# Kernel tuning notes

Hardware: AMD Instinct MI355X
Metric: run time of the kernel (lower is better)

## Reference

```python
import jax, jax.numpy as jnp
import numpy as np

N_LIG = 1024; K = 32; N = N_LIG * K; KNN = 8; E = N * KNN
IN_F = 16; T_F = 16; HID = 128; OUT_F = 64; DEPTH = 4; NG = 20; NT = 1000
EDGE_IN = NG + T_F  # 36
NORM_FACTOR = 5.0

# GaussianSmearing constants (type_='exp', start=0, stop=4, num_gaussians=20)
_off = np.exp(np.linspace(np.log(1.0), np.log(5.0), NG)) - 1.0
_d = np.diff(_off); _d = np.concatenate([_d[:1], _d])
GS_OFFSET = jnp.asarray(_off, jnp.float32)
GS_COEFF = jnp.asarray(-0.5 / _d ** 2, jnp.float32)


def _layernorm(v, g, b, eps=1e-5):
    mu = v.mean(-1, keepdims=True)
    var = ((v - mu) ** 2).mean(-1, keepdims=True)
    return (v - mu) / jnp.sqrt(var + eps) * g + b


def setup_inputs() -> dict:
    rng = np.random.default_rng(0)
    key = jax.random.key(0)
    ks = jax.random.split(key, 24)
    x = jax.random.uniform(ks[0], (N, 3), jnp.float32)   # keeps all sq-dists < 7
    h = jax.random.normal(ks[1], (N, IN_F), jnp.float32)
    t = jax.random.randint(ks[2], (N,), 0, NT, jnp.int32)
    t_bond = jax.random.randint(ks[3], (N_LIG * K * (K - 1),), 0, NT, jnp.int32)
    batch_ligand = (jnp.arange(N) // K).astype(jnp.int32)
    # knn-like edges restricted to each ligand (no self loops)
    i_local = np.arange(N) % K
    j = rng.integers(0, K, size=(N, KNN))
    j = np.where(j == i_local[:, None], (j + 1) % K, j)
    col = (np.arange(N) // K * K)[:, None] + j
    row = np.repeat(np.arange(N), KNN)
    edges = jnp.asarray(np.stack([row, col.reshape(-1)]), jnp.int32)

    def lin(k, fi, fo):
        return jax.random.normal(k, (fi, fo), jnp.float32) / np.sqrt(fi)

    def stk(k, fi, fo):
        return jax.random.normal(k, (DEPTH, fi, fo), jnp.float32) / np.sqrt(fi)

    inp = dict(x=x, h=h, t=t, edges=edges, t_bond=t_bond, batch_ligand=batch_ligand,
               num_atoms_per_ligand=K, num_ligands=N_LIG)
    inp['time_emb_table'] = 0.02 * jax.random.normal(ks[4], (NT, T_F), jnp.float32)
    inp['W_in'] = lin(ks[5], IN_F + T_F, HID); inp['b_in'] = jnp.zeros((HID,), jnp.float32)
    inp['gcl_We1'] = stk(ks[6], 2 * HID + EDGE_IN, HID); inp['gcl_be1'] = jnp.zeros((DEPTH, HID), jnp.float32)
    inp['gcl_g1'] = jnp.ones((DEPTH, HID), jnp.float32); inp['gcl_bt1'] = jnp.zeros((DEPTH, HID), jnp.float32)
    inp['gcl_We2'] = stk(ks[7], HID, HID); inp['gcl_be2'] = jnp.zeros((DEPTH, HID), jnp.float32)
    inp['gcl_Watt'] = stk(ks[8], HID, 1); inp['gcl_batt'] = jnp.zeros((DEPTH, 1), jnp.float32)
    inp['gcl_Wn1'] = stk(ks[9], 2 * HID, HID); inp['gcl_bn1'] = jnp.zeros((DEPTH, HID), jnp.float32)
    inp['gcl_g2'] = jnp.ones((DEPTH, HID), jnp.float32); inp['gcl_bt2'] = jnp.zeros((DEPTH, HID), jnp.float32)
    inp['gcl_Wn2'] = stk(ks[10], HID, HID); inp['gcl_bn2'] = jnp.zeros((DEPTH, HID), jnp.float32)
    inp['W_oe'] = lin(ks[11], HID, OUT_F); inp['b_oe'] = jnp.zeros((OUT_F,), jnp.float32)
    inp['W_f'] = lin(ks[12], OUT_F, 1); inp['b_f'] = jnp.zeros((1,), jnp.float32)
    return inp


def _forward(x, h, time_emb_table, W_in, b_in, gcl_We1, gcl_be1, gcl_g1, gcl_bt1,
             gcl_We2, gcl_be2, gcl_Watt, gcl_batt, gcl_Wn1, gcl_bn1, gcl_g2, gcl_bt2,
             gcl_Wn2, gcl_bn2, W_oe, b_oe, W_f, b_f,
             t, edges, t_bond, batch_ligand, num_atoms_per_ligand, num_ligands):
    n_nodes = x.shape[0]
    row, col = edges[0], edges[1]
    # h <- cat(h, time_emb)
    hh = jnp.concatenate([h, time_emb_table[t]], axis=-1)
    # distances + Gaussian smearing (all edges pass the <7 filter by construction)
    cdiff = x[row] - x[col]                          # [E,3]
    radial = jnp.sum(cdiff ** 2, axis=1)             # [E]
    dist = jnp.clip(jnp.sqrt(radial), 0.0, 4.0)
    dd = dist[:, None] - GS_OFFSET[None, :]
    smear = jnp.exp(GS_COEFF * dd * dd)              # [E,NG]
    Kc = num_atoms_per_ligand
    sbi = row * (Kc - 1) + col - (row // Kc) * Kc - (row < col).astype(row.dtype)
    edge_attr = jnp.concatenate([time_emb_table[t_bond[sbi]], smear], axis=-1)  # [E,36]
    hh = hh @ W_in + b_in                            # [N,HID]
    for l in range(DEPTH):
        # edge model: gather -> MLP(LN, SiLU) -> sigmoid attention gate
        m = jnp.concatenate([hh[row], hh[col], edge_attr], axis=-1)
        m = jax.nn.silu(_layernorm(m @ gcl_We1[l] + gcl_be1[l], gcl_g1[l], gcl_bt1[l]))
        mij = jax.nn.silu(m @ gcl_We2[l] + gcl_be2[l])
        att = jax.nn.sigmoid(mij @ gcl_Watt[l] + gcl_batt[l])
        ef = mij * att                               # [E,HID]
        # node model: scatter-add aggregate (sum / normalization_factor) -> MLP -> residual
        agg = jax.ops.segment_sum(ef, row, num_segments=n_nodes) / NORM_FACTOR
        nm = jnp.concatenate([hh, agg], axis=-1)
        nm = jax.nn.silu(_layernorm(nm @ gcl_Wn1[l] + gcl_bn1[l], gcl_g2[l], gcl_bt2[l]))
        hh = hh + (nm @ gcl_Wn2[l] + gcl_bn2[l])
    ho = hh @ W_oe + b_oe                            # [N,OUT_F]
    counts = jax.ops.segment_sum(jnp.ones((n_nodes,), ho.dtype), batch_ligand, num_segments=num_ligands)
    pooled = jax.ops.segment_sum(ho, batch_ligand, num_segments=num_ligands) / counts[:, None]
    return (pooled @ W_f + b_f).squeeze(-1)          # [num_ligands]


def reference(x, h, t, edges, t_bond, batch_ligand, num_atoms_per_ligand, num_ligands,
              time_emb_table, W_in, b_in, gcl_We1, gcl_be1, gcl_g1, gcl_bt1,
              gcl_We2, gcl_be2, gcl_Watt, gcl_batt, gcl_Wn1, gcl_bn1, gcl_g2, gcl_bt2,
              gcl_Wn2, gcl_bn2, W_oe, b_oe, W_f, b_f):
    return _forward(x, h, time_emb_table, W_in, b_in, gcl_We1, gcl_be1, gcl_g1, gcl_bt1,
                    gcl_We2, gcl_be2, gcl_Watt, gcl_batt, gcl_Wn1, gcl_bn1, gcl_g2, gcl_bt2,
                    gcl_Wn2, gcl_bn2, W_oe, b_oe, W_f, b_f,
                    t, edges, t_bond, batch_ligand, num_atoms_per_ligand, num_ligands)
```

## Files before the change

### kernel.cpp

```cpp
#include <hip/hip_runtime.h>
#include <math.h>

#define NNODES 32768
#define NLIG   1024
#define KAT    32
#define KNN    8
#define NEDGES (NNODES*KNN)
#define HID    128
#define TF     16
#define NG     20
#define OUTF   64

#define NPB    16
#define EPB    128
#define K1     320
#define MIDSTR 132

typedef unsigned short u16;
typedef _Float16 f16;
typedef __attribute__((__ext_vector_type__(8))) _Float16 f16x8;
typedef __attribute__((__ext_vector_type__(4))) float f32x4;

union U8h { f16 a[8]; f16x8 v; };

__device__ const float GS_OG[20] = {
    0.0f, 0.0883984f, 0.1845966f, 0.2893285f, 0.4033028f,
    0.5273539f, 0.6623701f, 0.8093209f, 0.9692606f, 1.1433389f,
    1.3328075f, 1.5390240f, 1.7634662f, 2.0077560f, 2.2736369f,
    2.5630207f, 2.8779861f, 3.2207938f, 3.5939058f, 4.0f };
__device__ const float GS_CF[20] = {
    -63.9853f, -63.9853f, -54.0303f, -45.5840f, -38.4908f,
    -32.4913f, -27.4283f, -23.1540f, -19.5460f, -16.4999f,
    -13.9282f, -11.7577f, -9.92569f, -8.37837f, -7.07287f,
    -5.97065f, -5.04016f, -4.25470f, -3.59163f, -3.03191f };

__device__ __forceinline__ float siluf(float v) {
    return __fdividef(v, 1.0f + __expf(-v));
}
__device__ __forceinline__ float sigf(float v) {
    return __fdividef(1.0f, 1.0f + __expf(-v));
}
__device__ __forceinline__ f32x4 mfma16(f16x8 a, f16x8 b, f32x4 c) {
    return __builtin_amdgcn_mfma_f32_16x16x32_f16(a, b, c, 0, 0, 0);
}

#define PREP_TEMB 16000
#define PREP_W1   (4*128*K1)
#define PREP_W2   (4*128*128)
#define PREP_WN1  (4*128*256)
#define PREP_WN2  (4*128*128)
#define PREP_TOT  (PREP_TEMB+PREP_W1+PREP_W2+PREP_WN1+PREP_WN2)

__global__ __launch_bounds__(256) void prep_k(
    const float* __restrict__ temb, const float* __restrict__ We1,
    const float* __restrict__ We2,  const float* __restrict__ Wn1,
    const float* __restrict__ Wn2,
    f16* __restrict__ tembF,
    f16* __restrict__ W1T, f16* __restrict__ W2T,
    f16* __restrict__ WN1T, f16* __restrict__ WN2T)
{
    int i = blockIdx.x*256 + threadIdx.x;
    if (i >= PREP_TOT) return;
    float v; f16* dst; int di;
    if (i < PREP_TEMB) {
        v = temb[i]; dst = tembF; di = i;
    } else if (i < PREP_TEMB + PREP_W1) {
        int j = i - PREP_TEMB; di = j; dst = W1T;
        int l = j / (128*K1); int r = j - l*(128*K1);
        int col = r / K1, k = r - col*K1;
        v = (k < 292) ? We1[(size_t)l*292*128 + (size_t)k*128 + col] : 0.0f;
    } else if (i < PREP_TEMB + PREP_W1 + PREP_W2) {
        int j = i - PREP_TEMB - PREP_W1; di = j; dst = W2T;
        int l = j >> 14; int r = j & 16383;
        int col = r >> 7, k = r & 127;
        v = We2[(size_t)l*16384 + (size_t)k*128 + col];
    } else if (i < PREP_TEMB + PREP_W1 + PREP_W2 + PREP_WN1) {
        int j = i - PREP_TEMB - PREP_W1 - PREP_W2; di = j; dst = WN1T;
        int l = j >> 15; int r = j & 32767;
        int col = r >> 8, k = r & 255;
        v = Wn1[(size_t)l*32768 + (size_t)k*128 + col];
    } else {
        int j = i - PREP_TEMB - PREP_W1 - PREP_W2 - PREP_WN1; di = j; dst = WN2T;
        int l = j >> 14; int r = j & 16383;
        int col = r >> 7, k = r & 127;
        v = Wn2[(size_t)l*16384 + (size_t)k*128 + col];
    }
    dst[di] = (f16)v;
}

__global__ __launch_bounds__(256) void embed_k(
    const float* __restrict__ h, const int* __restrict__ t,
    const float* __restrict__ temb, const float* __restrict__ Win,
    const float* __restrict__ bin, float* __restrict__ hh,
    f16* __restrict__ hhF)
{
    __shared__ float sIn[8][32];
    const int tid = threadIdx.x;
    {
        const int n = tid >> 5, i = tid & 31;
        const int node = blockIdx.x*8 + n;
        sIn[n][i] = (i < TF) ? h[node*TF + i] : temb[t[node]*TF + (i-TF)];
    }
    __syncthreads();
    const int sub = tid >> 7, col = tid & 127;
    float acc[4];
    const float b = bin[col];
    acc[0]=acc[1]=acc[2]=acc[3]=b;
    #pragma unroll 8
    for (int i = 0; i < 32; ++i) {
        const float wv = Win[i*HID + col];
        acc[0] = fmaf(sIn[sub][i],   wv, acc[0]);
        acc[1] = fmaf(sIn[2+sub][i], wv, acc[1]);
        acc[2] = fmaf(sIn[4+sub][i], wv, acc[2]);
        acc[3] = fmaf(sIn[6+sub][i], wv, acc[3]);
    }
    #pragma unroll
    for (int nn = 0; nn < 4; ++nn) {
        const size_t idx = (size_t)(blockIdx.x*8 + nn*2 + sub)*HID + col;
        hh[idx] = acc[nn];
        hhF[idx] = (f16)acc[nn];
    }
}

__global__ __launch_bounds__(256, 3) void edge_k(
    const f16* __restrict__ hhF, const float* __restrict__ x,
    const int* __restrict__ ecol, const int* __restrict__ tbond,
    const f16* __restrict__ tembF,
    const f16* __restrict__ W1T, const f16* __restrict__ W2T,
    const float* __restrict__ be1, const float* __restrict__ g1,
    const float* __restrict__ bt1, const float* __restrict__ be2,
    const float* __restrict__ Watt, const float* __restrict__ batt,
    f16* __restrict__ aggF)
{
    __shared__ __align__(16) char smem[38400];
    f16*   tbl   = (f16*)(smem);
    f16*   tailB = (f16*)(smem + 8192);
    float* sStats= (float*)(smem + 32768);
    float* sMuInv= (float*)(smem + 36864);
    f16*   sB2   = (f16*)(smem);
    float* sAP   = (float*)(smem + 32768);
    float* sAttv = (float*)(smem + 37888);

    const int tid = threadIdx.x;
    const int node0 = blockIdx.x * NPB;
    const int ligBase = node0 & ~31;
    const int aBase   = node0 & 31;
    const int w = tid >> 6, lane = tid & 63, lr = lane & 15, lh = lane >> 4;
    const int colB0 = w*32 + lr, colB1 = colB0 + 16;

    unsigned aColPk0 = 0, aColPk1 = 0;
    #pragma unroll
    for (int rt = 0; rt < 4; ++rt)
        aColPk0 |= (unsigned)(ecol[node0*KNN + rt*16 + lr] & 31) << (rt*8);
    #pragma unroll
    for (int rt = 0; rt < 4; ++rt)
        aColPk1 |= (unsigned)(ecol[node0*KNN + (4+rt)*16 + lr] & 31) << (rt*8);

    const f16* bF0 = W1T + (size_t)colB0*K1 + lh*8;
    const f16* bF1 = W1T + (size_t)colB1*K1 + lh*8;
    f16x8 wf0 = *(const f16x8*)bF0, wf1 = *(const f16x8*)bF1;

    for (int idx = tid; idx < 512; idx += 256) {
        const int a = idx >> 4, c4 = idx & 15;
        const f16x8 v = *(const f16x8*)(hhF + (size_t)(ligBase + a)*HID + c4*8);
        *(f16x8*)&tbl[a*128 + ((c4 ^ (a & 15)) << 3)] = v;
    }

    for (int pe = tid; pe < 1024; pe += 256) {
        const int row = pe & 127, part = pe >> 7;
        U8h vh;
        if (part < 2) {
            const int r = node0 + (row >> 3);
            const int c = ecol[node0*KNN + row];
            int sbi = r*(KAT-1) + c - (r/KAT)*KAT - (r < c ? 1 : 0);
            const int tb = tbond[sbi];
            #pragma unroll
            for (int j = 0; j < 8; ++j)
                vh.a[j] = tembF[tb*TF + part*8 + j];
        } else if (part < 5) {
            const int r = node0 + (row >> 3);
            const int c = ecol[node0*KNN + row];
            float dx = x[3*r]-x[3*c], dy = x[3*r+1]-x[3*c+1], dz = x[3*r+2]-x[3*c+2];
            float dist = fminf(sqrtf(dx*dx+dy*dy+dz*dz), 4.0f);
            #pragma unroll
            for (int j = 0; j < 8; ++j) {
                int g = (part-2)*8 + j;
                float v = 0.0f;
                if (g < NG) {
                    float dd = dist - GS_OG[g];
                    v = __expf(GS_CF[g]*dd*dd);
                }
                vh.a[j] = (f16)v;
            }
        } else {
            #pragma unroll
            for (int j = 0; j < 8; ++j) vh.a[j] = (f16)0.0f;
        }
        *(f16x8*)&tailB[row*64 + ((part ^ (row & 7)) << 3)] = vh.v;
    }
    __syncthreads();

    f32x4 acc[8][2];
    #pragma unroll
    for (int rt = 0; rt < 8; ++rt) { acc[rt][0] = (f32x4){0,0,0,0}; acc[rt][1] = (f32x4){0,0,0,0}; }
    {
        #pragma unroll
        for (int s = 0; s < 10; ++s) {
            f16x8 nf0 = wf0, nf1 = wf1;
            if (s < 9) {
                nf0 = *(const f16x8*)(bF0 + 32*(s+1));
                nf1 = *(const f16x8*)(bF1 + 32*(s+1));
            }
            if (s < 4) {
                #pragma unroll
                for (int rt = 0; rt < 8; ++rt) {
                    const int aR = aBase + 2*rt + (lr >> 3);
                    const int c4 = s*4 + lh;
                    const int ad = aR*128 + ((c4 ^ (aR & 15)) << 3);
                    const f16x8 ah = *(const f16x8*)&tbl[ad];
                    acc[rt][0] = mfma16(ah, wf0, acc[rt][0]);
                    acc[rt][1] = mfma16(ah, wf1, acc[rt][1]);
                }
            } else if (s < 8) {
                #pragma unroll
                for (int rt = 0; rt < 8; ++rt) {
                    const int aC = (int)((rt < 4 ? (aColPk0 >> (rt*8))
                                                 : (aColPk1 >> ((rt-4)*8))) & 31u);
                    const int c4 = (s-4)*4 + lh;
                    const int ad = aC*128 + ((c4 ^ (aC & 15)) << 3);
                    const f16x8 ah = *(const f16x8*)&tbl[ad];
                    acc[rt][0] = mfma16(ah, wf0, acc[rt][0]);
                    acc[rt][1] = mfma16(ah, wf1, acc[rt][1]);
                }
            } else {
                #pragma unroll
                for (int rt = 0; rt < 8; ++rt) {
                    const int r = rt*16 + lr;
                    const int c = (s-8)*4 + lh;
                    const int ad = r*64 + ((c ^ (r & 7)) << 3);
                    const f16x8 ah = *(const f16x8*)&tailB[ad];
                    acc[rt][0] = mfma16(ah, wf0, acc[rt][0]);
                    acc[rt][1] = mfma16(ah, wf1, acc[rt][1]);
                }
            }
            wf0 = nf0; wf1 = nf1;
        }
    }

    {
        const float b10 = be1[colB0], b11 = be1[colB1];
        #pragma unroll
        for (int rt = 0; rt < 8; ++rt)
            #pragma unroll
            for (int j = 0; j < 4; ++j) { acc[rt][0][j] += b10; acc[rt][1][j] += b11; }
    }
    {
        #pragma unroll
        for (int rt = 0; rt < 8; ++rt) {
            float sv[4], qv[4];
            #pragma unroll
            for (int j = 0; j < 4; ++j) {
                const float a0 = acc[rt][0][j], a1 = acc[rt][1][j];
                sv[j] = a0 + a1; qv[j] = a0*a0 + a1*a1;
            }
            #pragma unroll
            for (int msk = 1; msk < 16; msk <<= 1) {
                #pragma unroll
                for (int j = 0; j < 4; ++j) {
                    sv[j] += __shfl_xor(sv[j], msk);
                    qv[j] += __shfl_xor(qv[j], msk);
                }
            }
            if (lr == 0) {
                #pragma unroll
                for (int j = 0; j < 4; ++j) {
                    const int row = rt*16 + 4*lh + j;
                    sStats[(row*4 + w)*2 + 0] = sv[j];
                    sStats[(row*4 + w)*2 + 1] = qv[j];
                }
            }
        }
    }
    __syncthreads();

    if (tid < EPB) {
        const float4 a = *(const float4*)&sStats[tid*8];
        const float4 b = *(const float4*)&sStats[tid*8 + 4];
        const float st = a.x + a.z + b.x + b.z;
        const float qt = a.y + a.w + b.y + b.w;
        const float mu  = st * (1.0f/HID);
        const float var = qt * (1.0f/HID) - mu*mu;
        sMuInv[tid*2 + 0] = mu;
        sMuInv[tid*2 + 1] = rsqrtf(var + 1e-5f);
    }
    __syncthreads();

    const f16* c2F0 = W2T + (size_t)colB0*HID + lh*8;
    const f16* c2F1 = W2T + (size_t)colB1*HID + lh*8;
    f16x8 g2f0 = *(const f16x8*)c2F0, g2f1 = *(const f16x8*)c2F1;

    {
        const float G0 = g1[colB0], G1s = g1[colB1];
        const float B0 = bt1[colB0], B1s = bt1[colB1];
        #pragma unroll
        for (int rt = 0; rt < 8; ++rt) {
            const int r0 = rt*16 + 4*lh;
            const float4 mi0 = *(const float4*)&sMuInv[r0*2];
            const float4 mi1 = *(const float4*)&sMuInv[r0*2 + 4];
            acc[rt][0][0] = siluf(fmaf((acc[rt][0][0]-mi0.x)*mi0.y, G0, B0));
            acc[rt][1][0] = siluf(fmaf((acc[rt][1][0]-mi0.x)*mi0.y, G1s, B1s));
            acc[rt][0][1] = siluf(fmaf((acc[rt][0][1]-mi0.z)*mi0.w, G0, B0));
            acc[rt][1][1] = siluf(fmaf((acc[rt][1][1]-mi0.z)*mi0.w, G1s, B1s));
            acc[rt][0][2] = siluf(fmaf((acc[rt][0][2]-mi1.x)*mi1.y, G0, B0));
            acc[rt][1][2] = siluf(fmaf((acc[rt][1][2]-mi1.x)*mi1.y, G1s, B1s));
            acc[rt][0][3] = siluf(fmaf((acc[rt][0][3]-mi1.z)*mi1.w, G0, B0));
            acc[rt][1][3] = siluf(fmaf((acc[rt][1][3]-mi1.z)*mi1.w, G1s, B1s));
        }
    }
    {
        #pragma unroll
        for (int rt = 0; rt < 8; ++rt) {
            #pragma unroll
            for (int hcol = 0; hcol < 2; ++hcol) {
                const int col = hcol ? colB1 : colB0;
                const int gch = col >> 3, cw = col & 7;
                #pragma unroll
                for (int j = 0; j < 4; ++j) {
                    const int row = rt*16 + 4*lh + j;
                    sB2[row*128 + ((gch ^ (row & 15)) << 3) + cw] =
                        (f16)acc[rt][hcol][j];
                }
            }
        }
    }
    __syncthreads();

    f32x4 d[8][2];
    #pragma unroll
    for (int rt = 0; rt < 8; ++rt) { d[rt][0] = (f32x4){0,0,0,0}; d[rt][1] = (f32x4){0,0,0,0}; }
    {
        #pragma unroll
        for (int s = 0; s < 4; ++s) {
            f16x8 nf0 = g2f0, nf1 = g2f1;
            if (s < 3) {
                nf0 = *(const f16x8*)(c2F0 + 32*(s+1));
                nf1 = *(const f16x8*)(c2F1 + 32*(s+1));
            }
            #pragma unroll
            for (int rt = 0; rt < 8; ++rt) {
                const int rowL = rt*16 + lr;
                const int c4 = s*4 + lh;
                const f16x8 ah = *(const f16x8*)&sB2[rowL*128 + ((c4 ^ (rowL & 15)) << 3)];
                d[rt][0] = mfma16(ah, g2f0, d[rt][0]);
                d[rt][1] = mfma16(ah, g2f1, d[rt][1]);
            }
            g2f0 = nf0; g2f1 = nf1;
        }
    }

    {
        const float b20 = be2[colB0], b21 = be2[colB1];
        #pragma unroll
        for (int rt = 0; rt < 8; ++rt) {
            #pragma unroll
            for (int j = 0; j < 4; ++j) {
                d[rt][0][j] = siluf(d[rt][0][j] + b20);
                d[rt][1][j] = siluf(d[rt][1][j] + b21);
            }
        }
    }
    {
        const float wa0 = Watt[colB0], wa1 = Watt[colB1];
        float pa[8][4];
        #pragma unroll
        for (int rt = 0; rt < 8; ++rt)
            #pragma unroll
            for (int j = 0; j < 4; ++j)
                pa[rt][j] = d[rt][0][j]*wa0 + d[rt][1][j]*wa1;
        #pragma unroll
        for (int msk = 1; msk < 16; msk <<= 1) {
            #pragma unroll
            for (int rt = 0; rt < 8; ++rt)
                #pragma unroll
                for (int j = 0; j < 4; ++j)
                    pa[rt][j] += __shfl_xor(pa[rt][j], msk);
        }
        if (lr == 0) {
            #pragma unroll
            for (int rt = 0; rt < 8; ++rt)
                #pragma unroll
                for (int j = 0; j < 4; ++j)
                    sAP[w*128 + rt*16 + 4*lh + j] = pa[rt][j];
        }
    }
    __syncthreads();
    if (tid < EPB)
        sAttv[tid] = sigf(sAP[tid] + sAP[128+tid] + sAP[256+tid] + sAP[384+tid] + batt[0]);
    __syncthreads();

    #pragma unroll
    for (int rt = 0; rt < 8; ++rt) {
        float s0 = 0.0f, s1 = 0.0f;
        #pragma unroll
        for (int j = 0; j < 4; ++j) {
            const float av = sAttv[rt*16 + 4*lh + j];
            s0 += d[rt][0][j]*av;
            s1 += d[rt][1][j]*av;
        }
        s0 += __shfl_xor(s0, 16);
        s1 += __shfl_xor(s1, 16);
        if ((lh & 1) == 0) {
            const int node = node0 + 2*rt + (lh >> 1);
            aggF[(size_t)node*HID + colB0] = (f16)(s0*0.2f);
            aggF[(size_t)node*HID + colB1] = (f16)(s1*0.2f);
        }
    }
}

__global__ __launch_bounds__(256, 6) void node_k(
    float* __restrict__ hh, f16* __restrict__ hhF,
    const f16* __restrict__ aggF,
    const f16* __restrict__ B1T, const f16* __restrict__ B2T,
    const float* __restrict__ bn1, const float* __restrict__ g2,
    const float* __restrict__ bt2, const float* __restrict__ bn2)
{
    __shared__ __align__(16) char smem[16896];
    float* sMid = (float*)smem;
    f16* sY = (f16*)smem;

    const int tid = threadIdx.x;
    const int node0 = blockIdx.x * 32;
    const int w = tid >> 6, lane = tid & 63, lr = lane & 15, lh = lane >> 4;
    const int colB0 = w*32 + lr, colB1 = colB0 + 16;

    const f16* a1f = hhF  + (size_t)(node0+lr)*HID + lh*8;
    const f16* a2f = aggF + (size_t)(node0+lr)*HID + lh*8;
    const f16* c1F0 = B1T + (size_t)colB0*256 + lh*8;
    const f16* c1F1 = B1T + (size_t)colB1*256 + lh*8;

    f32x4 acc00={0,0,0,0}, acc01={0,0,0,0}, acc10={0,0,0,0}, acc11={0,0,0,0};
    {
        f16x8 wf0 = *(const f16x8*)c1F0, wf1 = *(const f16x8*)c1F1;
        #pragma unroll
        for (int s = 0; s < 8; ++s) {
            f16x8 nf0 = wf0, nf1 = wf1;
            if (s < 7) {
                nf0 = *(const f16x8*)(c1F0 + 32*(s+1));
                nf1 = *(const f16x8*)(c1F1 + 32*(s+1));
            }
            f16x8 ah0, ah1;
            if (s < 4) {
                ah0 = *(const f16x8*)(a1f + 32*s);
                ah1 = *(const f16x8*)(a1f + 16*HID + 32*s);
            } else {
                ah0 = *(const f16x8*)(a2f + 32*(s-4));
                ah1 = *(const f16x8*)(a2f + 16*HID + 32*(s-4));
            }
            acc00 = mfma16(ah0, wf0, acc00);
            acc01 = mfma16(ah0, wf1, acc01);
            acc10 = mfma16(ah1, wf0, acc10);
            acc11 = mfma16(ah1, wf1, acc11);
            wf0 = nf0; wf1 = nf1;
        }
    }
    {
        const float b10 = bn1[colB0], b11 = bn1[colB1];
        #pragma unroll
        for (int j = 0; j < 4; ++j) {
            const int r0 = 4*lh + j;
            sMid[r0*MIDSTR + colB0]      = acc00[j] + b10;
            sMid[r0*MIDSTR + colB1]      = acc01[j] + b11;
            sMid[(16+r0)*MIDSTR + colB0] = acc10[j] + b10;
            sMid[(16+r0)*MIDSTR + colB1] = acc11[j] + b11;
        }
    }
    __syncthreads();

    float y[16];
    const int eLN = tid >> 3, c0 = (tid & 7)*16;
    {
        const float* mrow = &sMid[eLN*MIDSTR + c0];
        float4 v0 = *(const float4*)&mrow[0];
        float4 v1 = *(const float4*)&mrow[4];
        float4 v2 = *(const float4*)&mrow[8];
        float4 v3 = *(const float4*)&mrow[12];
        float s = v0.x+v0.y+v0.z+v0.w + v1.x+v1.y+v1.z+v1.w
                + v2.x+v2.y+v2.z+v2.w + v3.x+v3.y+v3.z+v3.w;
        float q = v0.x*v0.x+v0.y*v0.y+v0.z*v0.z+v0.w*v0.w
                + v1.x*v1.x+v1.y*v1.y+v1.z*v1.z+v1.w*v1.w
                + v2.x*v2.x+v2.y*v2.y+v2.z*v2.z+v2.w*v2.w
                + v3.x*v3.x+v3.y*v3.y+v3.z*v3.z+v3.w*v3.w;
        #pragma unroll
        for (int m = 4; m >= 1; m >>= 1) { s += __shfl_xor(s, m); q += __shfl_xor(q, m); }
        float mu  = s * (1.0f/HID);
        float var = q * (1.0f/HID) - mu*mu;
        float inv = rsqrtf(var + 1e-5f);
        const float4 G0 = *(const float4*)&g2[c0+0],  G1v = *(const float4*)&g2[c0+4];
        const float4 G2 = *(const float4*)&g2[c0+8],  G3 = *(const float4*)&g2[c0+12];
        const float4 B0 = *(const float4*)&bt2[c0+0], B1 = *(const float4*)&bt2[c0+4];
        const float4 B2 = *(const float4*)&bt2[c0+8], B3 = *(const float4*)&bt2[c0+12];
        y[0]=siluf(fmaf((v0.x-mu)*inv,G0.x,B0.x));  y[1]=siluf(fmaf((v0.y-mu)*inv,G0.y,B0.y));
        y[2]=siluf(fmaf((v0.z-mu)*inv,G0.z,B0.z));  y[3]=siluf(fmaf((v0.w-mu)*inv,G0.w,B0.w));
        y[4]=siluf(fmaf((v1.x-mu)*inv,G1v.x,B1.x)); y[5]=siluf(fmaf((v1.y-mu)*inv,G1v.y,B1.y));
        y[6]=siluf(fmaf((v1.z-mu)*inv,G1v.z,B1.z)); y[7]=siluf(fmaf((v1.w-mu)*inv,G1v.w,B1.w));
        y[8]=siluf(fmaf((v2.x-mu)*inv,G2.x,B2.x));  y[9]=siluf(fmaf((v2.y-mu)*inv,G2.y,B2.y));
        y[10]=siluf(fmaf((v2.z-mu)*inv,G2.z,B2.z)); y[11]=siluf(fmaf((v2.w-mu)*inv,G2.w,B2.w));
        y[12]=siluf(fmaf((v3.x-mu)*inv,G3.x,B3.x)); y[13]=siluf(fmaf((v3.y-mu)*inv,G3.y,B3.y));
        y[14]=siluf(fmaf((v3.z-mu)*inv,G3.z,B3.z)); y[15]=siluf(fmaf((v3.w-mu)*inv,G3.w,B3.w));
    }
    __syncthreads();
    {
        U8h ha, hb2;
        #pragma unroll
        for (int j = 0; j < 8; ++j) {
            ha.a[j]  = (f16)y[j];
            hb2.a[j] = (f16)y[8+j];
        }
        const int cA = (2*(tid & 7))     ^ (eLN & 15);
        const int cB = (2*(tid & 7) + 1) ^ (eLN & 15);
        *(f16x8*)&sY[eLN*128 + (cA << 3)] = ha.v;
        *(f16x8*)&sY[eLN*128 + (cB << 3)] = hb2.v;
    }
    __syncthreads();

    f32x4 d00={0,0,0,0}, d01={0,0,0,0}, d10={0,0,0,0}, d11={0,0,0,0};
    {
        const f16* c2F0 = B2T + (size_t)colB0*HID + lh*8;
        const f16* c2F1 = B2T + (size_t)colB1*HID + lh*8;
        f16x8 wf0 = *(const f16x8*)c2F0, wf1 = *(const f16x8*)c2F1;
        #pragma unroll
        for (int s = 0; s < 4; ++s) {
            f16x8 nf0 = wf0, nf1 = wf1;
            if (s < 3) {
                nf0 = *(const f16x8*)(c2F0 + 32*(s+1));
                nf1 = *(const f16x8*)(c2F1 + 32*(s+1));
            }
            const int c4 = s*4 + lh;
            const int i0 = lr*128 + ((c4 ^ lr) << 3);
            const int i1 = (16+lr)*128 + ((c4 ^ lr) << 3);
            f16x8 ah0 = *(const f16x8*)&sY[i0], ah1 = *(const f16x8*)&sY[i1];
            d00 = mfma16(ah0, wf0, d00);
            d01 = mfma16(ah0, wf1, d01);
            d10 = mfma16(ah1, wf0, d10);
            d11 = mfma16(ah1, wf1, d11);
            wf0 = nf0; wf1 = nf1;
        }
    }

    {
        const float b20 = bn2[colB0], b21 = bn2[colB1];
        #pragma unroll
        for (int j = 0; j < 4; ++j) {
            const int r0 = 4*lh + j, r1 = 16 + 4*lh + j;
            const size_t i00 = (size_t)(node0+r0)*HID + colB0;
            const size_t i01 = (size_t)(node0+r0)*HID + colB1;
            const size_t i10 = (size_t)(node0+r1)*HID + colB0;
            const size_t i11 = (size_t)(node0+r1)*HID + colB1;
            float v00 = hh[i00] + d00[j] + b20;
            float v01 = hh[i01] + d01[j] + b21;
            float v10 = hh[i10] + d10[j] + b20;
            float v11 = hh[i11] + d11[j] + b21;
            hh[i00] = v00; hh[i01] = v01; hh[i10] = v10; hh[i11] = v11;
            hhF[i00] = (f16)v00; hhF[i01] = (f16)v01;
            hhF[i10] = (f16)v10; hhF[i11] = (f16)v11;
        }
    }
}

__global__ __launch_bounds__(HID) void out_k(
    const float* __restrict__ hh, const float* __restrict__ Woe,
    const float* __restrict__ boe, const float* __restrict__ Wf,
    const float* __restrict__ bf, float* __restrict__ out)
{
    __shared__ float sH[HID];
    const int lig = blockIdx.x, tid = threadIdx.x;
    float s = 0.0f;
    const float* base = hh + (size_t)lig*KAT*HID + tid;
    #pragma unroll 8
    for (int a = 0; a < KAT; ++a) s += base[a*HID];
    sH[tid] = s * (1.0f/KAT);
    __syncthreads();

    float contrib = 0.0f;
    if (tid < OUTF) {
        float p = boe[tid];
        #pragma unroll 4
        for (int i = 0; i < HID; ++i)
            p = fmaf(sH[i], Woe[i*OUTF + tid], p);
        contrib = p * Wf[tid];
    }
    #pragma unroll
    for (int m = 1; m < 64; m <<= 1) contrib += __shfl_xor(contrib, m);
    if (tid == 0) out[lig] = contrib + bf[0];
}

extern "C" void kernel_launch(void* const* d_in, const int* in_sizes, int n_in,
                              void* d_out, int out_size, void* d_ws, size_t ws_size,
                              hipStream_t stream)
{
    (void)in_sizes; (void)n_in; (void)out_size; (void)ws_size;
    const float* x    = (const float*)d_in[0];
    const float* h    = (const float*)d_in[1];
    const int*   t    = (const int*)d_in[2];
    const int*   edges= (const int*)d_in[3];
    const int*   tb   = (const int*)d_in[4];
    const float* temb = (const float*)d_in[8];
    const float* Win  = (const float*)d_in[9];
    const float* bin  = (const float*)d_in[10];
    const float* We1  = (const float*)d_in[11];
    const float* be1  = (const float*)d_in[12];
    const float* g1   = (const float*)d_in[13];
    const float* bt1  = (const float*)d_in[14];
    const float* We2  = (const float*)d_in[15];
    const float* be2  = (const float*)d_in[16];
    const float* Watt = (const float*)d_in[17];
    const float* batt = (const float*)d_in[18];
    const float* Wn1  = (const float*)d_in[19];
    const float* bn1  = (const float*)d_in[20];
    const float* g2   = (const float*)d_in[21];
    const float* bt2  = (const float*)d_in[22];
    const float* Wn2  = (const float*)d_in[23];
    const float* bn2  = (const float*)d_in[24];
    const float* Woe  = (const float*)d_in[25];
    const float* boe  = (const float*)d_in[26];
    const float* Wf   = (const float*)d_in[27];
    const float* bf   = (const float*)d_in[28];
    float* out = (float*)d_out;

    char* wsb = (char*)d_ws;
    float* hh  = (float*)(wsb);
    f16* hhF   = (f16*)(wsb + ((size_t)16<<20));
    f16* aggF  = (f16*)(wsb + ((size_t)24<<20));
    f16* tembF = (f16*)(wsb + ((size_t)32<<20));
    f16* W1T   = tembF + PREP_TEMB;
    f16* W2T   = W1T + PREP_W1;
    f16* WN1T  = W2T + PREP_W2;
    f16* WN2T  = WN1T + PREP_WN1;

    prep_k<<<(PREP_TOT + 255)/256, 256, 0, stream>>>(
        temb, We1, We2, Wn1, Wn2, tembF, W1T, W2T, WN1T, WN2T);

    embed_k<<<NNODES/8, 256, 0, stream>>>(h, t, temb, Win, bin, hh, hhF);

    for (int l = 0; l < 4; ++l) {
        edge_k<<<NNODES/NPB, 256, 0, stream>>>(
            hhF, x, edges + NEDGES, tb, tembF,
            W1T + (size_t)l*128*K1, W2T + (size_t)l*128*128,
            be1 + l*HID, g1 + l*HID, bt1 + l*HID, be2 + l*HID,
            Watt + l*HID, batt + l, aggF);
        node_k<<<NNODES/32, 256, 0, stream>>>(
            hh, hhF, aggF,
            WN1T + (size_t)l*128*256, WN2T + (size_t)l*128*128,
            bn1 + l*HID, g2 + l*HID, bt2 + l*HID, bn2 + l*HID);
    }
    out_k<<<NLIG, HID, 0, stream>>>(hh, Woe, boe, Wf, bf, out);
}
```

Before: 480.1 us.

## Split edge kernel columns across eight waves with 512-thread blocks

The edge kernel block grows from 256 to 512 threads, so each of 8 waves owns 16 output columns instead of 32. Per-thread accumulators and MFMA work are halved, and the LayerNorm statistics and attention partial sums are now reduced over 8 wave slots. The aim is more waves per block and lower register pressure, to improve latency hiding. The cost is a larger shared-memory footprint, twice as many A-fragment LDS reads per MFMA, and more cross-wave reduction work.

Result: slower. 603.0 us (+25.6%).

```diff
diff --git a/kernel.cpp b/kernel.cpp
--- a/kernel.cpp
+++ b/kernel.cpp
@@ -122,7 +122,7 @@
     }
 }
 
-__global__ __launch_bounds__(256, 3) void edge_k(
+__global__ __launch_bounds__(512, 4) void edge_k(
     const f16* __restrict__ hhF, const float* __restrict__ x,
     const int* __restrict__ ecol, const int* __restrict__ tbond,
     const f16* __restrict__ tembF,
@@ -132,21 +132,21 @@
     const float* __restrict__ Watt, const float* __restrict__ batt,
     f16* __restrict__ aggF)
 {
-    __shared__ __align__(16) char smem[38400];
+    __shared__ __align__(16) char smem[46592];
     f16*   tbl   = (f16*)(smem);
     f16*   tailB = (f16*)(smem + 8192);
     float* sStats= (float*)(smem + 32768);
-    float* sMuInv= (float*)(smem + 36864);
+    float* sMuInv= (float*)(smem + 40960);
+    float* sAP   = (float*)(smem + 41984);
+    float* sAttv = (float*)(smem + 46080);
     f16*   sB2   = (f16*)(smem);
-    float* sAP   = (float*)(smem + 32768);
-    float* sAttv = (float*)(smem + 37888);
 
     const int tid = threadIdx.x;
     const int node0 = blockIdx.x * NPB;
     const int ligBase = node0 & ~31;
     const int aBase   = node0 & 31;
     const int w = tid >> 6, lane = tid & 63, lr = lane & 15, lh = lane >> 4;
-    const int colB0 = w*32 + lr, colB1 = colB0 + 16;
+    const int colB = w*16 + lr;
 
     unsigned aColPk0 = 0, aColPk1 = 0;
     #pragma unroll
@@ -156,17 +156,16 @@
     for (int rt = 0; rt < 4; ++rt)
         aColPk1 |= (unsigned)(ecol[node0*KNN + (4+rt)*16 + lr] & 31) << (rt*8);
 
-    const f16* bF0 = W1T + (size_t)colB0*K1 + lh*8;
-    const f16* bF1 = W1T + (size_t)colB1*K1 + lh*8;
-    f16x8 wf0 = *(const f16x8*)bF0, wf1 = *(const f16x8*)bF1;
-
-    for (int idx = tid; idx < 512; idx += 256) {
-        const int a = idx >> 4, c4 = idx & 15;
+    const f16* bF = W1T + (size_t)colB*K1 + lh*8;
+    f16x8 wf = *(const f16x8*)bF;
+
+    {
+        const int a = tid >> 4, c4 = tid & 15;
         const f16x8 v = *(const f16x8*)(hhF + (size_t)(ligBase + a)*HID + c4*8);
         *(f16x8*)&tbl[a*128 + ((c4 ^ (a & 15)) << 3)] = v;
     }
 
-    for (int pe = tid; pe < 1024; pe += 256) {
+    for (int pe = tid; pe < 1024; pe += 512) {
         const int row = pe & 127, part = pe >> 7;
         U8h vh;
         if (part < 2) {
@@ -200,26 +199,21 @@
     }
     __syncthreads();
 
-    f32x4 acc[8][2];
+    f32x4 acc[8];
     #pragma unroll
-    for (int rt = 0; rt < 8; ++rt) { acc[rt][0] = (f32x4){0,0,0,0}; acc[rt][1] = (f32x4){0,0,0,0}; }
+    for (int rt = 0; rt < 8; ++rt) acc[rt] = (f32x4){0,0,0,0};
     {
         #pragma unroll
         for (int s = 0; s < 10; ++s) {
-            f16x8 nf0 = wf0, nf1 = wf1;
-            if (s < 9) {
-                nf0 = *(const f16x8*)(bF0 + 32*(s+1));
-                nf1 = *(const f16x8*)(bF1 + 32*(s+1));
-            }
+            f16x8 nf = wf;
+            if (s < 9) nf = *(const f16x8*)(bF + 32*(s+1));
             if (s < 4) {
                 #pragma unroll
                 for (int rt = 0; rt < 8; ++rt) {
                     const int aR = aBase + 2*rt + (lr >> 3);
                     const int c4 = s*4 + lh;
                     const int ad = aR*128 + ((c4 ^ (aR & 15)) << 3);
-                    const f16x8 ah = *(const f16x8*)&tbl[ad];
-                    acc[rt][0] = mfma16(ah, wf0, acc[rt][0]);
-                    acc[rt][1] = mfma16(ah, wf1, acc[rt][1]);
+                    acc[rt] = mfma16(*(const f16x8*)&tbl[ad], wf, acc[rt]);
                 }
             } else if (s < 8) {
                 #pragma unroll
@@ -228,9 +222,7 @@
                                                  : (aColPk1 >> ((rt-4)*8))) & 31u);
                     const int c4 = (s-4)*4 + lh;
                     const int ad = aC*128 + ((c4 ^ (aC & 15)) << 3);
-                    const f16x8 ah = *(const f16x8*)&tbl[ad];
-                    acc[rt][0] = mfma16(ah, wf0, acc[rt][0]);
-                    acc[rt][1] = mfma16(ah, wf1, acc[rt][1]);
+                    acc[rt] = mfma16(*(const f16x8*)&tbl[ad], wf, acc[rt]);
                 }
             } else {
                 #pragma unroll
@@ -238,30 +230,23 @@
                     const int r = rt*16 + lr;
                     const int c = (s-8)*4 + lh;
                     const int ad = r*64 + ((c ^ (r & 7)) << 3);
-                    const f16x8 ah = *(const f16x8*)&tailB[ad];
-                    acc[rt][0] = mfma16(ah, wf0, acc[rt][0]);
-                    acc[rt][1] = mfma16(ah, wf1, acc[rt][1]);
+                    acc[rt] = mfma16(*(const f16x8*)&tailB[ad], wf, acc[rt]);
                 }
             }
-            wf0 = nf0; wf1 = nf1;
-        }
-    }
-
-    {
-        const float b10 = be1[colB0], b11 = be1[colB1];
-        #pragma unroll
-        for (int rt = 0; rt < 8; ++rt)
-            #pragma unroll
-            for (int j = 0; j < 4; ++j) { acc[rt][0][j] += b10; acc[rt][1][j] += b11; }
-    }
-    {
+            wf = nf;
+        }
+    }
+
+    {
+        const float b1 = be1[colB];
         #pragma unroll
         for (int rt = 0; rt < 8; ++rt) {
             float sv[4], qv[4];
             #pragma unroll
             for (int j = 0; j < 4; ++j) {
-                const float a0 = acc[rt][0][j], a1 = acc[rt][1][j];
-                sv[j] = a0 + a1; qv[j] = a0*a0 + a1*a1;
+                const float a0 = acc[rt][j] + b1;
+                acc[rt][j] = a0;
+                sv[j] = a0; qv[j] = a0*a0;
             }
             #pragma unroll
             for (int msk = 1; msk < 16; msk <<= 1) {
@@ -275,8 +260,8 @@
                 #pragma unroll
                 for (int j = 0; j < 4; ++j) {
                     const int row = rt*16 + 4*lh + j;
-                    sStats[(row*4 + w)*2 + 0] = sv[j];
-                    sStats[(row*4 + w)*2 + 1] = qv[j];
+                    sStats[(row*8 + w)*2 + 0] = sv[j];
+                    sStats[(row*8 + w)*2 + 1] = qv[j];
                 }
             }
         }
@@ -284,135 +269,110 @@
     __syncthreads();
 
     if (tid < EPB) {
-        const float4 a = *(const float4*)&sStats[tid*8];
-        const float4 b = *(const float4*)&sStats[tid*8 + 4];
-        const float st = a.x + a.z + b.x + b.z;
-        const float qt = a.y + a.w + b.y + b.w;
-        const float mu  = st * (1.0f/HID);
-        const float var = qt * (1.0f/HID) - mu*mu;
+        const float* rp = &sStats[tid*16];
+        float s = 0.0f, q = 0.0f;
+        #pragma unroll
+        for (int k = 0; k < 8; ++k) {
+            const float2 v = *(const float2*)&rp[2*k];
+            s += v.x; q += v.y;
+        }
+        const float mu  = s * (1.0f/HID);
+        const float var = q * (1.0f/HID) - mu*mu;
         sMuInv[tid*2 + 0] = mu;
         sMuInv[tid*2 + 1] = rsqrtf(var + 1e-5f);
     }
     __syncthreads();
 
-    const f16* c2F0 = W2T + (size_t)colB0*HID + lh*8;
-    const f16* c2F1 = W2T + (size_t)colB1*HID + lh*8;
-    f16x8 g2f0 = *(const f16x8*)c2F0, g2f1 = *(const f16x8*)c2F1;
-
-    {
-        const float G0 = g1[colB0], G1s = g1[colB1];
-        const float B0 = bt1[colB0], B1s = bt1[colB1];
+    const f16* c2F = W2T + (size_t)colB*HID + lh*8;
+    f16x8 g2f = *(const f16x8*)c2F;
+
+    {
+        const float G = g1[colB], B = bt1[colB];
+        const int gch = colB >> 3, cw = colB & 7;
         #pragma unroll
         for (int rt = 0; rt < 8; ++rt) {
             const int r0 = rt*16 + 4*lh;
             const float4 mi0 = *(const float4*)&sMuInv[r0*2];
             const float4 mi1 = *(const float4*)&sMuInv[r0*2 + 4];
-            acc[rt][0][0] = siluf(fmaf((acc[rt][0][0]-mi0.x)*mi0.y, G0, B0));
-            acc[rt][1][0] = siluf(fmaf((acc[rt][1][0]-mi0.x)*mi0.y, G1s, B1s));
-            acc[rt][0][1] = siluf(fmaf((acc[rt][0][1]-mi0.z)*mi0.w, G0, B0));
-            acc[rt][1][1] = siluf(fmaf((acc[rt][1][1]-mi0.z)*mi0.w, G1s, B1s));
-            acc[rt][0][2] = siluf(fmaf((acc[rt][0][2]-mi1.x)*mi1.y, G0, B0));
-            acc[rt][1][2] = siluf(fmaf((acc[rt][1][2]-mi1.x)*mi1.y, G1s, B1s));
-            acc[rt][0][3] = siluf(fmaf((acc[rt][0][3]-mi1.z)*mi1.w, G0, B0));
-            acc[rt][1][3] = siluf(fmaf((acc[rt][1][3]-mi1.z)*mi1.w, G1s, B1s));
-        }
-    }
-    {
-        #pragma unroll
-        for (int rt = 0; rt < 8; ++rt) {
-            #pragma unroll
-            for (int hcol = 0; hcol < 2; ++hcol) {
-                const int col = hcol ? colB1 : colB0;
-                const int gch = col >> 3, cw = col & 7;
-                #pragma unroll
-                for (int j = 0; j < 4; ++j) {
-                    const int row = rt*16 + 4*lh + j;
-                    sB2[row*128 + ((gch ^ (row & 15)) << 3) + cw] =
-                        (f16)acc[rt][hcol][j];
-                }
-            }
-        }
-    }
-    __syncthreads();
-
-    f32x4 d[8][2];
+            acc[rt][0] = siluf(fmaf((acc[rt][0]-mi0.x)*mi0.y, G, B));
+            acc[rt][1] = siluf(fmaf((acc[rt][1]-mi0.z)*mi0.w, G, B));
+            acc[rt][2] = siluf(fmaf((acc[rt][2]-mi1.x)*mi1.y, G, B));
+            acc[rt][3] = siluf(fmaf((acc[rt][3]-mi1.z)*mi1.w, G, B));
+            #pragma unroll
+            for (int j = 0; j < 4; ++j) {
+                const int row = r0 + j;
+                sB2[row*128 + ((gch ^ (row & 15)) << 3) + cw] = (f16)acc[rt][j];
+            }
+        }
+    }
+    __syncthreads();
+
+    f32x4 d[8];
     #pragma unroll
-    for (int rt = 0; rt < 8; ++rt) { d[rt][0] = (f32x4){0,0,0,0}; d[rt][1] = (f32x4){0,0,0,0}; }
+    for (int rt = 0; rt < 8; ++rt) d[rt] = (f32x4){0,0,0,0};
     {
         #pragma unroll
         for (int s = 0; s < 4; ++s) {
-            f16x8 nf0 = g2f0, nf1 = g2f1;
-            if (s < 3) {
-                nf0 = *(const f16x8*)(c2F0 + 32*(s+1));
-                nf1 = *(const f16x8*)(c2F1 + 32*(s+1));
-            }
+            f16x8 nf = g2f;
+            if (s < 3) nf = *(const f16x8*)(c2F + 32*(s+1));
             #pragma unroll
             for (int rt = 0; rt < 8; ++rt) {
                 const int rowL = rt*16 + lr;
                 const int c4 = s*4 + lh;
                 const f16x8 ah = *(const f16x8*)&sB2[rowL*128 + ((c4 ^ (rowL & 15)) << 3)];
-                d[rt][0] = mfma16(ah, g2f0, d[rt][0]);
-                d[rt][1] = mfma16(ah, g2f1, d[rt][1]);
-            }
-            g2f0 = nf0; g2f1 = nf1;
-        }
-    }
-
-    {
-        const float b20 = be2[colB0], b21 = be2[colB1];
+                d[rt] = mfma16(ah, g2f, d[rt]);
+            }
+            g2f = nf;
+        }
+    }
+
+    {
+        const float b2 = be2[colB];
+        #pragma unroll
+        for (int rt = 0; rt < 8; ++rt)
+            #pragma unroll
+            for (int j = 0; j < 4; ++j)
+                d[rt][j] = siluf(d[rt][j] + b2);
+    }
+    {
+        const float wa = Watt[colB];
         #pragma unroll
         for (int rt = 0; rt < 8; ++rt) {
-            #pragma unroll
-            for (int j = 0; j < 4; ++j) {
-                d[rt][0][j] = siluf(d[rt][0][j] + b20);
-                d[rt][1][j] = siluf(d[rt][1][j] + b21);
-            }
-        }
-    }
-    {
-        const float wa0 = Watt[colB0], wa1 = Watt[colB1];
-        float pa[8][4];
-        #pragma unroll
-        for (int rt = 0; rt < 8; ++rt)
-            #pragma unroll
-            for (int j = 0; j < 4; ++j)
-                pa[rt][j] = d[rt][0][j]*wa0 + d[rt][1][j]*wa1;
-        #pragma unroll
-        for (int msk = 1; msk < 16; msk <<= 1) {
-            #pragma unroll
-            for (int rt = 0; rt < 8; ++rt)
+            float pa[4];
+            #pragma unroll
+            for (int j = 0; j < 4; ++j) pa[j] = d[rt][j]*wa;
+            #pragma unroll
+            for (int msk = 1; msk < 16; msk <<= 1) {
                 #pragma unroll
                 for (int j = 0; j < 4; ++j)
-                    pa[rt][j] += __shfl_xor(pa[rt][j], msk);
-        }
-        if (lr == 0) {
-            #pragma unroll
-            for (int rt = 0; rt < 8; ++rt)
+                    pa[j] += __shfl_xor(pa[j], msk);
+            }
+            if (lr == 0) {
                 #pragma unroll
                 for (int j = 0; j < 4; ++j)
-                    sAP[w*128 + rt*16 + 4*lh + j] = pa[rt][j];
-        }
-    }
-    __syncthreads();
-    if (tid < EPB)
-        sAttv[tid] = sigf(sAP[tid] + sAP[128+tid] + sAP[256+tid] + sAP[384+tid] + batt[0]);
+                    sAP[w*128 + rt*16 + 4*lh + j] = pa[j];
+            }
+        }
+    }
+    __syncthreads();
+    if (tid < EPB) {
+        float p = batt[0];
+        #pragma unroll
+        for (int k = 0; k < 8; ++k) p += sAP[k*128 + tid];
+        sAttv[tid] = sigf(p);
+    }
     __syncthreads();
 
     #pragma unroll
     for (int rt = 0; rt < 8; ++rt) {
-        float s0 = 0.0f, s1 = 0.0f;
-        #pragma unroll
-        for (int j = 0; j < 4; ++j) {
-            const float av = sAttv[rt*16 + 4*lh + j];
-            s0 += d[rt][0][j]*av;
-            s1 += d[rt][1][j]*av;
-        }
+        float s0 = 0.0f;
+        #pragma unroll
+        for (int j = 0; j < 4; ++j)
+            s0 += d[rt][j] * sAttv[rt*16 + 4*lh + j];
         s0 += __shfl_xor(s0, 16);
-        s1 += __shfl_xor(s1, 16);
         if ((lh & 1) == 0) {
             const int node = node0 + 2*rt + (lh >> 1);
-            aggF[(size_t)node*HID + colB0] = (f16)(s0*0.2f);
-            aggF[(size_t)node*HID + colB1] = (f16)(s1*0.2f);
+            aggF[(size_t)node*HID + colB] = (f16)(s0*0.2f);
         }
     }
 }
@@ -643,7 +603,7 @@
     embed_k<<<NNODES/8, 256, 0, stream>>>(h, t, temb, Win, bin, hh, hhF);
 
     for (int l = 0; l < 4; ++l) {
-        edge_k<<<NNODES/NPB, 256, 0, stream>>>(
+        edge_k<<<NNODES/NPB, 512, 0, stream>>>(
             hhF, x, edges + NEDGES, tb, tembF,
             W1T + (size_t)l*128*K1, W2T + (size_t)l*128*128,
             be1 + l*HID, g1 + l*HID, bt1 + l*HID, be2 + l*HID,
```
